# Performance work log

Measured on AMD Instinct MI355X. Metric: run time of the kernel, lower is better.

The kernel has to match this reference:

```python
import jax, jax.numpy as jnp
import numpy as np

HEADS = 16
DIM_HEAD = 64
EPS = 1e-8
MASK_VALUE = -np.finfo(np.float32).max


def rotate_half(x):
    # x: [..., rot_dim]; split into two halves (j=2 grouping) and rotate
    x1, x2 = jnp.split(x.reshape(*x.shape[:-1], 2, x.shape[-1] // 2), 2, axis=-2)
    x1 = x1.squeeze(-2)
    x2 = x2.squeeze(-2)
    return jnp.concatenate((-x2, x1), axis=-1)


def apply_rotary_pos_emb(t, freqs):
    # t: [b, h, n, d], freqs: [n, rot_dim]
    rot_dim = freqs.shape[-1]
    t_rot, t_pass = t[..., :rot_dim], t[..., rot_dim:]
    t_rot = t_rot * jnp.cos(freqs) + rotate_half(t_rot) * jnp.sin(freqs)
    return jnp.concatenate((t_rot, t_pass), axis=-1)


def setup_inputs() -> dict:
    key = jax.random.key(0)
    ks = jax.random.split(key, 6)
    b, n, dim = 2, 2048, 1024
    inner = HEADS * DIM_HEAD
    rot_dim = 32
    return {
        "x": jax.random.normal(ks[0], (b, n, dim), jnp.float32),
        "freqs": jax.random.normal(ks[1], (n, rot_dim), jnp.float32),
        "gamma": jnp.ones((dim,), jnp.float32),
        "Wq": jax.random.normal(ks[2], (dim, inner), jnp.float32) * (dim ** -0.5),
        "Wkv": jax.random.normal(ks[3], (dim, 2 * inner), jnp.float32) * (dim ** -0.5),
        "Wo": jax.random.normal(ks[4], (inner, dim), jnp.float32) * (inner ** -0.5),
        "bo": jnp.zeros((dim,), jnp.float32),
    }


def reference(x, freqs, gamma, Wq, Wkv, Wo, bo):
    b, n, dim = x.shape
    scale = DIM_HEAD ** -0.5

    # RMSNorm (norm-based formulation, matching the torch code)
    norm = jnp.linalg.norm(x, axis=-1, keepdims=True) * (dim ** -0.5)
    xn = x / jnp.maximum(norm, EPS) * gamma

    q = xn @ Wq                      # [b, n, h*d]
    kv = xn @ Wkv                    # [b, n, 2*h*d]
    k, v = jnp.split(kv, 2, axis=-1)

    def to_heads(t):
        return t.reshape(b, n, HEADS, DIM_HEAD).transpose(0, 2, 1, 3)  # [b,h,n,d]

    q, k, v = map(to_heads, (q, k, v))
    q = q * scale

    q = apply_rotary_pos_emb(q, freqs)
    k = apply_rotary_pos_emb(k, freqs)

    sim = jnp.einsum('bhid,bhjd->bhij', q, k)
    causal_mask = jnp.triu(jnp.ones((n, n), bool), k=1)
    sim = jnp.where(causal_mask, MASK_VALUE, sim)

    attn = jax.nn.softmax(sim, axis=-1)
    out = jnp.einsum('bhij,bhjd->bhid', attn, v)
    out = out.transpose(0, 2, 1, 3).reshape(b, n, HEADS * DIM_HEAD)
    return out @ Wo + bo
```

## Files before the change

### kernel.cpp

```cpp
#include <hip/hip_runtime.h>
#include <hip/hip_bf16.h>
#include <math.h>

typedef short s8 __attribute__((ext_vector_type(8)));
typedef float f4 __attribute__((ext_vector_type(4)));

#define HEADS 16
#define DHEAD 64
#define NSEQ 2048
#define BATCH 2
#define DIM 1024
#define ROT 32

static __device__ __forceinline__ unsigned short f2bf(float f) {
    union { float f; unsigned int u; } v; v.f = f;
    unsigned int u = v.u;
    unsigned int r = (u + 0x7FFFu + ((u >> 16) & 1u)) >> 16;
    return (unsigned short)r;
}

static __device__ __forceinline__ unsigned int cvt_pk_bf16(float lo, float hi) {
    unsigned int r;
    asm volatile("v_cvt_pk_bf16_f32 %0, %1, %2" : "=v"(r) : "v"(lo), "v"(hi));
    return r;
}

static __device__ __forceinline__ void gload_lds16(
        const unsigned short* g, unsigned short* l) {
    __builtin_amdgcn_global_load_lds(
        (const __attribute__((address_space(1))) void*)g,
        (__attribute__((address_space(3))) void*)l,
        16, 0, 0);
}

__global__ __launch_bounds__(256) void transpose_f32_bf16(
        const float* __restrict__ in, unsigned short* __restrict__ out,
        int K, int N) {
    __shared__ float tile[32][33];
    int n0 = blockIdx.x * 32, k0 = blockIdx.y * 32;
    int tx = threadIdx.x, ty = threadIdx.y;
    #pragma unroll
    for (int j = 0; j < 32; j += 8)
        tile[ty + j][tx] = in[(size_t)(k0 + ty + j) * N + n0 + tx];
    __syncthreads();
    #pragma unroll
    for (int j = 0; j < 32; j += 8)
        out[(size_t)(n0 + ty + j) * K + k0 + tx] = f2bf(tile[tx][ty + j]);
}

__global__ __launch_bounds__(256) void freqs_prep(
        const float* __restrict__ freqs, float* __restrict__ cs) {
    int i = blockIdx.x * 256 + threadIdx.x;
    int npos = i >> 6, j = i & 63;
    int q = j >> 4;
    int fi = (q >> 1) * 16 + (j & 15);
    float f = freqs[npos * ROT + fi];
    cs[i] = (q & 1) ? sinf(f) : cosf(f);
}

__global__ __launch_bounds__(256) void rmsnorm_kernel(
        const float* __restrict__ x, const float* __restrict__ gamma,
        unsigned short* __restrict__ xn) {
    int row = blockIdx.x;
    int tid = threadIdx.x;
    float4 v = ((const float4*)(x + (size_t)row * DIM))[tid];
    float ss = v.x * v.x + v.y * v.y + v.z * v.z + v.w * v.w;
    #pragma unroll
    for (int m = 1; m < 64; m <<= 1) ss += __shfl_xor(ss, m, 64);
    __shared__ float wsum[4];
    int wave = tid >> 6;
    if ((tid & 63) == 0) wsum[wave] = ss;
    __syncthreads();
    float total = wsum[0] + wsum[1] + wsum[2] + wsum[3];
    float norm = sqrtf(total * (1.0f / DIM));
    float inv = 1.0f / fmaxf(norm, 1e-8f);
    float4 g = ((const float4*)gamma)[tid];
    ushort4 o;
    o.x = f2bf(v.x * inv * g.x);
    o.y = f2bf(v.y * inv * g.y);
    o.z = f2bf(v.z * inv * g.z);
    o.w = f2bf(v.w * inv * g.w);
    ((ushort4*)(xn + (size_t)row * DIM))[tid] = o;
}

static __device__ __forceinline__ void gemm_core64(
        const unsigned short* __restrict__ A, const unsigned short* __restrict__ BT,
        int bm0, int bn0, unsigned short* As, unsigned short* Bs, f4 acc[2][4]) {
    const int Kd = DIM;
    int tid = threadIdx.x, lane = tid & 63, w = tid >> 6;
    int wr = w >> 1, wc = w & 1;
    int r16 = lane & 15, g8 = 8 * (lane >> 4);
    int srow = lane >> 2, scol = (lane & 3) * 8;
    const unsigned short* Ag0 = A  + (size_t)(bm0 + w * 16 + srow) * Kd + scol;
    const unsigned short* Bg0 = BT + (size_t)(bn0 + (w * 2 + 0) * 16 + srow) * Kd + scol;
    const unsigned short* Bg1 = BT + (size_t)(bn0 + (w * 2 + 1) * 16 + srow) * Kd + scol;
    unsigned short* Al  = As + w * 512;
    unsigned short* Bl0 = Bs + (w * 2 + 0) * 512;
    unsigned short* Bl1 = Bs + (w * 2 + 1) * 512;
    const unsigned short* ar = As + (wr * 32 + r16) * 32 + g8;
    const unsigned short* br = Bs + (wc * 64 + r16) * 32 + g8;
    for (int k0 = 0; k0 < Kd; k0 += 32) {
        gload_lds16(Ag0 + k0, Al);
        gload_lds16(Bg0 + k0, Bl0);
        gload_lds16(Bg1 + k0, Bl1);
        __syncthreads();
        s8 a0 = *(const s8*)(ar);
        s8 a1 = *(const s8*)(ar + 512);
        s8 b0 = *(const s8*)(br);
        s8 b1 = *(const s8*)(br + 512);
        s8 b2 = *(const s8*)(br + 1024);
        s8 b3 = *(const s8*)(br + 1536);
        acc[0][0] = __builtin_amdgcn_mfma_f32_16x16x32_bf16(a0, b0, acc[0][0], 0, 0, 0);
        acc[0][1] = __builtin_amdgcn_mfma_f32_16x16x32_bf16(a0, b1, acc[0][1], 0, 0, 0);
        acc[0][2] = __builtin_amdgcn_mfma_f32_16x16x32_bf16(a0, b2, acc[0][2], 0, 0, 0);
        acc[0][3] = __builtin_amdgcn_mfma_f32_16x16x32_bf16(a0, b3, acc[0][3], 0, 0, 0);
        acc[1][0] = __builtin_amdgcn_mfma_f32_16x16x32_bf16(a1, b0, acc[1][0], 0, 0, 0);
        acc[1][1] = __builtin_amdgcn_mfma_f32_16x16x32_bf16(a1, b1, acc[1][1], 0, 0, 0);
        acc[1][2] = __builtin_amdgcn_mfma_f32_16x16x32_bf16(a1, b2, acc[1][2], 0, 0, 0);
        acc[1][3] = __builtin_amdgcn_mfma_f32_16x16x32_bf16(a1, b3, acc[1][3], 0, 0, 0);
        __syncthreads();
    }
}

__global__ __launch_bounds__(256) void gemm_q(
        const unsigned short* __restrict__ xn, const unsigned short* __restrict__ WqT,
        const float* __restrict__ cs, unsigned short* __restrict__ q_h) {
    __shared__ unsigned short As[64 * 32];
    __shared__ unsigned short Bs[128 * 32];
    f4 acc[2][4];
    #pragma unroll
    for (int m = 0; m < 2; ++m)
        #pragma unroll
        for (int n = 0; n < 4; ++n) acc[m][n] = 0.f;
    int bm0 = blockIdx.y * 64, bn0 = blockIdx.x * 128;
    gemm_core64(xn, WqT, bm0, bn0, As, Bs, acc);
    int lane = threadIdx.x & 63, w = threadIdx.x >> 6;
    int wr = w >> 1, wc = w & 1, g = lane >> 4, c0 = lane & 15;
    int h = 2 * blockIdx.x + wc;
    #pragma unroll
    for (int m = 0; m < 2; ++m)
        #pragma unroll
        for (int r = 0; r < 4; ++r) {
            int row = bm0 + wr * 32 + m * 16 + 4 * g + r;
            int b = row >> 11, npos = row & 2047;
            const float* csr = cs + npos * 64;
            float a0 = acc[m][0][r] * 0.125f;
            float a1 = acc[m][1][r] * 0.125f;
            float q0 = a0 * csr[c0] - a1 * csr[16 + c0];
            float q1 = a1 * csr[32 + c0] + a0 * csr[48 + c0];
            unsigned short* dst = q_h + ((size_t)(b * HEADS + h) * NSEQ + npos) * DHEAD;
            dst[c0]      = f2bf(q0);
            dst[16 + c0] = f2bf(q1);
            dst[32 + c0] = f2bf(acc[m][2][r] * 0.125f);
            dst[48 + c0] = f2bf(acc[m][3][r] * 0.125f);
        }
}

__global__ __launch_bounds__(256) void gemm_kv(
        const unsigned short* __restrict__ xn, const unsigned short* __restrict__ WkvT,
        const float* __restrict__ cs, unsigned short* __restrict__ k_h,
        unsigned short* __restrict__ v_t) {
    __shared__ unsigned short As[64 * 32];
    __shared__ unsigned short Bs[128 * 32];
    f4 acc[2][4];
    #pragma unroll
    for (int m = 0; m < 2; ++m)
        #pragma unroll
        for (int n = 0; n < 4; ++n) acc[m][n] = 0.f;
    int bm0 = blockIdx.y * 64, bn0 = blockIdx.x * 128;
    gemm_core64(xn, WkvT, bm0, bn0, As, Bs, acc);
    int lane = threadIdx.x & 63, w = threadIdx.x >> 6;
    int wr = w >> 1, wc = w & 1, g = lane >> 4, c0 = lane & 15;
    bool is_k = (blockIdx.x < 8);
    int h = 2 * (blockIdx.x & 7) + wc;
    if (is_k) {
        #pragma unroll
        for (int m = 0; m < 2; ++m)
            #pragma unroll
            for (int r = 0; r < 4; ++r) {
                int row = bm0 + wr * 32 + m * 16 + 4 * g + r;
                int b = row >> 11, npos = row & 2047;
                const float* csr = cs + npos * 64;
                float a0 = acc[m][0][r], a1 = acc[m][1][r];
                float k0v = a0 * csr[c0] - a1 * csr[16 + c0];
                float k1v = a1 * csr[32 + c0] + a0 * csr[48 + c0];
                unsigned short* dst = k_h + ((size_t)(b * HEADS + h) * NSEQ + npos) * DHEAD;
                dst[c0]      = f2bf(k0v);
                dst[16 + c0] = f2bf(k1v);
                dst[32 + c0] = f2bf(acc[m][2][r]);
                dst[48 + c0] = f2bf(acc[m][3][r]);
            }
    } else {
        #pragma unroll
        for (int m = 0; m < 2; ++m) {
            int row0 = bm0 + wr * 32 + m * 16 + 4 * g;
            int b = row0 >> 11, npos0 = row0 & 2047;
            unsigned short* vb = v_t + (size_t)(b * HEADS + h) * DHEAD * NSEQ;
            #pragma unroll
            for (int n = 0; n < 4; ++n) {
                uint2 pk;
                pk.x = cvt_pk_bf16(acc[m][n][0], acc[m][n][1]);
                pk.y = cvt_pk_bf16(acc[m][n][2], acc[m][n][3]);
                *(uint2*)(vb + (size_t)(n * 16 + c0) * NSEQ + npos0) = pk;
            }
        }
    }
}

#define PSTRIDE 72

static __device__ __forceinline__ void stage_kv64(
        const unsigned short* __restrict__ kb, const unsigned short* __restrict__ vb,
        int j0, unsigned short* Kd, unsigned short* Vd, int w, int lane) {
    int r8 = lane >> 3, c = lane & 7;
    int sc = c ^ r8;
    #pragma unroll
    for (int i = 0; i < 2; ++i) {
        int rb = (w * 2 + i) * 8;
        int r = rb + r8;
        gload_lds16(kb + (size_t)(j0 + r) * DHEAD + sc * 8, Kd + rb * DHEAD);
        gload_lds16(vb + (size_t)r * NSEQ + j0 + sc * 8,    Vd + rb * DHEAD);
    }
}

template<bool MASKT>
static __device__ __forceinline__ void attn_tile_lds(
        int j0, int q0, int g, int c0, int njt,
        const unsigned short* Kc, const unsigned short* Vc,
        s8 qf0, s8 qf1, unsigned short* plw,
        f4 o[4], float& m, float& l) {
    int sw = c0 & 7;
    int off0 = ((g ^ sw) << 3);
    int off1 = (((g + 4) ^ sw) << 3);
    f4 s[4];
    #pragma unroll
    for (int jt = 0; jt < 4; ++jt) {
        f4 acc; acc = 0.f;
        if (!MASKT || jt < njt) {
            const unsigned short* kp = Kc + (jt * 16 + c0) * DHEAD;
            s8 kf0 = *(const s8*)(kp + off0);
            s8 kf1 = *(const s8*)(kp + off1);
            acc = __builtin_amdgcn_mfma_f32_16x16x32_bf16(kf0, qf0, acc, 0, 0, 0);
            acc = __builtin_amdgcn_mfma_f32_16x16x32_bf16(kf1, qf1, acc, 0, 0, 0);
        }
        s[jt] = acc;
    }
    if (MASKT) {
        #pragma unroll
        for (int jt = 0; jt < 4; ++jt)
            #pragma unroll
            for (int r = 0; r < 4; ++r) {
                int j = j0 + jt * 16 + 4 * g + r;
                if (j > q0 + c0) s[jt][r] = -1e30f;
            }
    }
    f4 mv = s[0];
    #pragma unroll
    for (int jt = 1; jt < 4; ++jt)
        #pragma unroll
        for (int r = 0; r < 4; ++r) mv[r] = fmaxf(mv[r], s[jt][r]);
    float mx = fmaxf(fmaxf(mv[0], mv[1]), fmaxf(mv[2], mv[3]));
    mx = fmaxf(mx, __shfl_xor(mx, 16));
    mx = fmaxf(mx, __shfl_xor(mx, 32));
    if (__any(mx > m + 8.f)) {
        float mnew = fmaxf(m, mx);
        float alpha = __expf(m - mnew);
        l *= alpha;
        #pragma unroll
        for (int dc = 0; dc < 4; ++dc)
            #pragma unroll
            for (int r = 0; r < 4; ++r) o[dc][r] *= alpha;
        m = mnew;
    }
    float rs = 0.f;
    unsigned int* prow = (unsigned int*)(plw + c0 * PSTRIDE);
    #pragma unroll
    for (int jt = 0; jt < 4; ++jt) {
        f4 p;
        #pragma unroll
        for (int r = 0; r < 4; ++r) { p[r] = __expf(s[jt][r] - m); rs += p[r]; }
        uint2 pk;
        pk.x = cvt_pk_bf16(p[0], p[1]);
        pk.y = cvt_pk_bf16(p[2], p[3]);
        ((uint2*)prow)[jt * 4 + g] = pk;
    }
    rs += __shfl_xor(rs, 16);
    rs += __shfl_xor(rs, 32);
    l += rs;
    __builtin_amdgcn_sched_barrier(0);
    asm volatile("s_waitcnt lgkmcnt(0)" ::: "memory");
    __builtin_amdgcn_sched_barrier(0);
    const unsigned short* prd = plw + c0 * PSTRIDE + 8 * g;
    s8 pf0 = *(const s8*)(prd);
    s8 pf1 = *(const s8*)(prd + 32);
    bool hi_half = (!MASKT) || (njt > 2);
    #pragma unroll
    for (int dc = 0; dc < 4; ++dc) {
        const unsigned short* vp = Vc + (dc * 16 + c0) * DHEAD;
        s8 vf0 = *(const s8*)(vp + off0);
        o[dc] = __builtin_amdgcn_mfma_f32_16x16x32_bf16(vf0, pf0, o[dc], 0, 0, 0);
        if (hi_half) {
            s8 vf1 = *(const s8*)(vp + off1);
            o[dc] = __builtin_amdgcn_mfma_f32_16x16x32_bf16(vf1, pf1, o[dc], 0, 0, 0);
        }
    }
}

__global__ __launch_bounds__(256) void attn_kernel(
        const unsigned short* __restrict__ q_h, const unsigned short* __restrict__ k_h,
        const unsigned short* __restrict__ v_t, unsigned short* __restrict__ attn_out) {
    __shared__ unsigned short Ks[2][64 * DHEAD];
    __shared__ unsigned short Vs[2][64 * DHEAD];
    __shared__ unsigned short p_lds[4][16][PSTRIDE];
    int tid = threadIdx.x, lane = tid & 63, w = tid >> 6;
    int g = lane >> 4, c0 = lane & 15;
    int bid = blockIdx.x;
    int x = (bid >> 3) & 15;
    int bh = (bid & 7) + ((bid >> 7) << 3);
    const unsigned short* qb = q_h + (size_t)bh * NSEQ * DHEAD;
    const unsigned short* kb = k_h + (size_t)bh * NSEQ * DHEAD;
    const unsigned short* vb = v_t + (size_t)bh * DHEAD * NSEQ;
    unsigned short* plw = &p_lds[w][0][0];
    int b = bh >> 4, h = bh & 15;
    for (int pass = 0; pass < 2; ++pass) {
        int qt = pass ? (31 - x) : x;
        int q0 = qt * 64 + w * 16;
        s8 qf0 = *(const s8*)(qb + (size_t)(q0 + c0) * DHEAD + 8 * g);
        s8 qf1 = *(const s8*)(qb + (size_t)(q0 + c0) * DHEAD + 32 + 8 * g);
        f4 o[4]; o[0] = 0.f; o[1] = 0.f; o[2] = 0.f; o[3] = 0.f;
        float m = -1e30f, l = 0.f;
        int nt = qt + 1;
        stage_kv64(kb, vb, 0, Ks[0], Vs[0], w, lane);
        __syncthreads();
        for (int t = 0; t < nt; ++t) {
            const unsigned short* Kc = Ks[t & 1];
            const unsigned short* Vc = Vs[t & 1];
            if (t + 1 < nt)
                stage_kv64(kb, vb, (t + 1) * 64, Ks[(t + 1) & 1], Vs[(t + 1) & 1], w, lane);
            if (t == nt - 1)
                attn_tile_lds<true>(t * 64, q0, g, c0, w + 1, Kc, Vc, qf0, qf1, plw, o, m, l);
            else
                attn_tile_lds<false>(t * 64, q0, g, c0, 4, Kc, Vc, qf0, qf1, plw, o, m, l);
            __syncthreads();
        }
        float invl = 1.0f / l;
        unsigned short* dst = attn_out + ((size_t)(b * NSEQ) + q0 + c0) * (HEADS * DHEAD) + h * DHEAD;
        #pragma unroll
        for (int dc = 0; dc < 4; ++dc) {
            uint2 pk;
            pk.x = cvt_pk_bf16(o[dc][0] * invl, o[dc][1] * invl);
            pk.y = cvt_pk_bf16(o[dc][2] * invl, o[dc][3] * invl);
            *(uint2*)(dst + dc * 16 + 4 * g) = pk;
        }
    }
}

__global__ __launch_bounds__(256) void gemm_o(
        const unsigned short* __restrict__ attn, const unsigned short* __restrict__ WoT,
        const float* __restrict__ bo, float* __restrict__ out) {
    __shared__ unsigned short As[64 * 32];
    __shared__ unsigned short Bs[128 * 32];
    f4 acc[2][4];
    #pragma unroll
    for (int m = 0; m < 2; ++m)
        #pragma unroll
        for (int n = 0; n < 4; ++n) acc[m][n] = 0.f;
    int bm0 = blockIdx.y * 64, bn0 = blockIdx.x * 128;
    gemm_core64(attn, WoT, bm0, bn0, As, Bs, acc);
    int lane = threadIdx.x & 63, w = threadIdx.x >> 6;
    int wr = w >> 1, wc = w & 1, g = lane >> 4, c0 = lane & 15;
    #pragma unroll
    for (int m = 0; m < 2; ++m)
        #pragma unroll
        for (int r = 0; r < 4; ++r) {
            int row = bm0 + wr * 32 + m * 16 + 4 * g + r;
            #pragma unroll
            for (int n = 0; n < 4; ++n) {
                int col = bn0 + wc * 64 + n * 16 + c0;
                out[(size_t)row * DIM + col] = acc[m][n][r] + bo[col];
            }
        }
}

extern "C" void kernel_launch(void* const* d_in, const int* in_sizes, int n_in,
                              void* d_out, int out_size, void* d_ws, size_t ws_size,
                              hipStream_t stream) {
    const float* x     = (const float*)d_in[0];
    const float* freqs = (const float*)d_in[1];
    const float* gamma = (const float*)d_in[2];
    const float* Wq    = (const float*)d_in[3];
    const float* Wkv   = (const float*)d_in[4];
    const float* Wo    = (const float*)d_in[5];
    const float* bo    = (const float*)d_in[6];
    float* out = (float*)d_out;

    char* ws = (char*)d_ws;
    unsigned short* xn   = (unsigned short*)(ws + 0);
    unsigned short* WqT  = (unsigned short*)(ws + 8388608);
    unsigned short* WkvT = (unsigned short*)(ws + 10485760);
    unsigned short* WoT  = (unsigned short*)(ws + 14680064);
    unsigned short* q_h  = (unsigned short*)(ws + 16777216);
    unsigned short* k_h  = (unsigned short*)(ws + 25165824);
    unsigned short* v_t  = (unsigned short*)(ws + 33554432);
    float*          cs   = (float*)(ws + 41943040);
    unsigned short* attn = xn;

    dim3 tb(32, 8);
    transpose_f32_bf16<<<dim3(32, 32), tb, 0, stream>>>(Wq,  WqT,  1024, 1024);
    transpose_f32_bf16<<<dim3(64, 32), tb, 0, stream>>>(Wkv, WkvT, 1024, 2048);
    transpose_f32_bf16<<<dim3(32, 32), tb, 0, stream>>>(Wo,  WoT,  1024, 1024);
    freqs_prep<<<512, 256, 0, stream>>>(freqs, cs);
    rmsnorm_kernel<<<4096, 256, 0, stream>>>(x, gamma, xn);
    gemm_q <<<dim3(8, 64),  256, 0, stream>>>(xn, WqT, cs, q_h);
    gemm_kv<<<dim3(16, 64), 256, 0, stream>>>(xn, WkvT, cs, k_h, v_t);
    attn_kernel<<<512, 256, 0, stream>>>(q_h, k_h, v_t, attn);
    gemm_o <<<dim3(8, 64),  256, 0, stream>>>(attn, WoT, bo, out);
}
```

Measured before the change: 139.0 us.

## Use 128x128 GEMM tiles, exp2 softmax with folded log2e, one q-tile per attention block

```diff
diff --git a/kernel.cpp b/kernel.cpp
--- a/kernel.cpp
+++ b/kernel.cpp
@@ -11,6 +11,7 @@
 #define BATCH 2
 #define DIM 1024
 #define ROT 32
+#define QSCALE 0.18033688011112042f
 
 static __device__ __forceinline__ unsigned short f2bf(float f) {
     union { float f; unsigned int u; } v; v.f = f;
@@ -83,41 +84,40 @@
     ((ushort4*)(xn + (size_t)row * DIM))[tid] = o;
 }
 
-static __device__ __forceinline__ void gemm_core64(
+static __device__ __forceinline__ void gemm_core128(
         const unsigned short* __restrict__ A, const unsigned short* __restrict__ BT,
-        int bm0, int bn0, unsigned short* As, unsigned short* Bs, f4 acc[2][4]) {
+        int bm0, int bn0, unsigned short* As, unsigned short* Bs, f4 acc[4][4]) {
     const int Kd = DIM;
     int tid = threadIdx.x, lane = tid & 63, w = tid >> 6;
     int wr = w >> 1, wc = w & 1;
     int r16 = lane & 15, g8 = 8 * (lane >> 4);
-    int srow = lane >> 2, scol = (lane & 3) * 8;
-    const unsigned short* Ag0 = A  + (size_t)(bm0 + w * 16 + srow) * Kd + scol;
-    const unsigned short* Bg0 = BT + (size_t)(bn0 + (w * 2 + 0) * 16 + srow) * Kd + scol;
-    const unsigned short* Bg1 = BT + (size_t)(bn0 + (w * 2 + 1) * 16 + srow) * Kd + scol;
-    unsigned short* Al  = As + w * 512;
-    unsigned short* Bl0 = Bs + (w * 2 + 0) * 512;
-    unsigned short* Bl1 = Bs + (w * 2 + 1) * 512;
-    const unsigned short* ar = As + (wr * 32 + r16) * 32 + g8;
+    int sr = lane >> 2, sc = (lane & 3) * 8;
+    const unsigned short* Ag0 = A  + (size_t)(bm0 +      w * 16 + sr) * Kd + sc;
+    const unsigned short* Ag1 = A  + (size_t)(bm0 + 64 + w * 16 + sr) * Kd + sc;
+    const unsigned short* Bg0 = BT + (size_t)(bn0 +      w * 16 + sr) * Kd + sc;
+    const unsigned short* Bg1 = BT + (size_t)(bn0 + 64 + w * 16 + sr) * Kd + sc;
+    unsigned short* Al0 = As + (w * 16) * 32;
+    unsigned short* Al1 = As + (64 + w * 16) * 32;
+    unsigned short* Bl0 = Bs + (w * 16) * 32;
+    unsigned short* Bl1 = Bs + (64 + w * 16) * 32;
+    const unsigned short* ar = As + (wr * 64 + r16) * 32 + g8;
     const unsigned short* br = Bs + (wc * 64 + r16) * 32 + g8;
     for (int k0 = 0; k0 < Kd; k0 += 32) {
-        gload_lds16(Ag0 + k0, Al);
+        gload_lds16(Ag0 + k0, Al0);
+        gload_lds16(Ag1 + k0, Al1);
         gload_lds16(Bg0 + k0, Bl0);
         gload_lds16(Bg1 + k0, Bl1);
         __syncthreads();
-        s8 a0 = *(const s8*)(ar);
-        s8 a1 = *(const s8*)(ar + 512);
-        s8 b0 = *(const s8*)(br);
-        s8 b1 = *(const s8*)(br + 512);
-        s8 b2 = *(const s8*)(br + 1024);
-        s8 b3 = *(const s8*)(br + 1536);
-        acc[0][0] = __builtin_amdgcn_mfma_f32_16x16x32_bf16(a0, b0, acc[0][0], 0, 0, 0);
-        acc[0][1] = __builtin_amdgcn_mfma_f32_16x16x32_bf16(a0, b1, acc[0][1], 0, 0, 0);
-        acc[0][2] = __builtin_amdgcn_mfma_f32_16x16x32_bf16(a0, b2, acc[0][2], 0, 0, 0);
-        acc[0][3] = __builtin_amdgcn_mfma_f32_16x16x32_bf16(a0, b3, acc[0][3], 0, 0, 0);
-        acc[1][0] = __builtin_amdgcn_mfma_f32_16x16x32_bf16(a1, b0, acc[1][0], 0, 0, 0);
-        acc[1][1] = __builtin_amdgcn_mfma_f32_16x16x32_bf16(a1, b1, acc[1][1], 0, 0, 0);
-        acc[1][2] = __builtin_amdgcn_mfma_f32_16x16x32_bf16(a1, b2, acc[1][2], 0, 0, 0);
-        acc[1][3] = __builtin_amdgcn_mfma_f32_16x16x32_bf16(a1, b3, acc[1][3], 0, 0, 0);
+        s8 a[4], b[4];
+        #pragma unroll
+        for (int m = 0; m < 4; ++m) a[m] = *(const s8*)(ar + m * 512);
+        #pragma unroll
+        for (int n = 0; n < 4; ++n) b[n] = *(const s8*)(br + n * 512);
+        #pragma unroll
+        for (int m = 0; m < 4; ++m)
+            #pragma unroll
+            for (int n = 0; n < 4; ++n)
+                acc[m][n] = __builtin_amdgcn_mfma_f32_16x16x32_bf16(a[m], b[n], acc[m][n], 0, 0, 0);
         __syncthreads();
     }
 }
@@ -125,34 +125,34 @@
 __global__ __launch_bounds__(256) void gemm_q(
         const unsigned short* __restrict__ xn, const unsigned short* __restrict__ WqT,
         const float* __restrict__ cs, unsigned short* __restrict__ q_h) {
-    __shared__ unsigned short As[64 * 32];
+    __shared__ unsigned short As[128 * 32];
     __shared__ unsigned short Bs[128 * 32];
-    f4 acc[2][4];
-    #pragma unroll
-    for (int m = 0; m < 2; ++m)
+    f4 acc[4][4];
+    #pragma unroll
+    for (int m = 0; m < 4; ++m)
         #pragma unroll
         for (int n = 0; n < 4; ++n) acc[m][n] = 0.f;
-    int bm0 = blockIdx.y * 64, bn0 = blockIdx.x * 128;
-    gemm_core64(xn, WqT, bm0, bn0, As, Bs, acc);
+    int bm0 = blockIdx.y * 128, bn0 = blockIdx.x * 128;
+    gemm_core128(xn, WqT, bm0, bn0, As, Bs, acc);
     int lane = threadIdx.x & 63, w = threadIdx.x >> 6;
     int wr = w >> 1, wc = w & 1, g = lane >> 4, c0 = lane & 15;
     int h = 2 * blockIdx.x + wc;
     #pragma unroll
-    for (int m = 0; m < 2; ++m)
+    for (int m = 0; m < 4; ++m)
         #pragma unroll
         for (int r = 0; r < 4; ++r) {
-            int row = bm0 + wr * 32 + m * 16 + 4 * g + r;
+            int row = bm0 + wr * 64 + m * 16 + 4 * g + r;
             int b = row >> 11, npos = row & 2047;
             const float* csr = cs + npos * 64;
-            float a0 = acc[m][0][r] * 0.125f;
-            float a1 = acc[m][1][r] * 0.125f;
+            float a0 = acc[m][0][r] * QSCALE;
+            float a1 = acc[m][1][r] * QSCALE;
             float q0 = a0 * csr[c0] - a1 * csr[16 + c0];
             float q1 = a1 * csr[32 + c0] + a0 * csr[48 + c0];
             unsigned short* dst = q_h + ((size_t)(b * HEADS + h) * NSEQ + npos) * DHEAD;
             dst[c0]      = f2bf(q0);
             dst[16 + c0] = f2bf(q1);
-            dst[32 + c0] = f2bf(acc[m][2][r] * 0.125f);
-            dst[48 + c0] = f2bf(acc[m][3][r] * 0.125f);
+            dst[32 + c0] = f2bf(acc[m][2][r] * QSCALE);
+            dst[48 + c0] = f2bf(acc[m][3][r] * QSCALE);
         }
 }
 
@@ -160,25 +160,25 @@
         const unsigned short* __restrict__ xn, const unsigned short* __restrict__ WkvT,
         const float* __restrict__ cs, unsigned short* __restrict__ k_h,
         unsigned short* __restrict__ v_t) {
-    __shared__ unsigned short As[64 * 32];
+    __shared__ unsigned short As[128 * 32];
     __shared__ unsigned short Bs[128 * 32];
-    f4 acc[2][4];
-    #pragma unroll
-    for (int m = 0; m < 2; ++m)
+    f4 acc[4][4];
+    #pragma unroll
+    for (int m = 0; m < 4; ++m)
         #pragma unroll
         for (int n = 0; n < 4; ++n) acc[m][n] = 0.f;
-    int bm0 = blockIdx.y * 64, bn0 = blockIdx.x * 128;
-    gemm_core64(xn, WkvT, bm0, bn0, As, Bs, acc);
+    int bm0 = blockIdx.y * 128, bn0 = blockIdx.x * 128;
+    gemm_core128(xn, WkvT, bm0, bn0, As, Bs, acc);
     int lane = threadIdx.x & 63, w = threadIdx.x >> 6;
     int wr = w >> 1, wc = w & 1, g = lane >> 4, c0 = lane & 15;
     bool is_k = (blockIdx.x < 8);
     int h = 2 * (blockIdx.x & 7) + wc;
     if (is_k) {
         #pragma unroll
-        for (int m = 0; m < 2; ++m)
+        for (int m = 0; m < 4; ++m)
             #pragma unroll
             for (int r = 0; r < 4; ++r) {
-                int row = bm0 + wr * 32 + m * 16 + 4 * g + r;
+                int row = bm0 + wr * 64 + m * 16 + 4 * g + r;
                 int b = row >> 11, npos = row & 2047;
                 const float* csr = cs + npos * 64;
                 float a0 = acc[m][0][r], a1 = acc[m][1][r];
@@ -192,8 +192,8 @@
             }
     } else {
         #pragma unroll
-        for (int m = 0; m < 2; ++m) {
-            int row0 = bm0 + wr * 32 + m * 16 + 4 * g;
+        for (int m = 0; m < 4; ++m) {
+            int row0 = bm0 + wr * 64 + m * 16 + 4 * g;
             int b = row0 >> 11, npos0 = row0 & 2047;
             unsigned short* vb = v_t + (size_t)(b * HEADS + h) * DHEAD * NSEQ;
             #pragma unroll
@@ -262,9 +262,9 @@
     float mx = fmaxf(fmaxf(mv[0], mv[1]), fmaxf(mv[2], mv[3]));
     mx = fmaxf(mx, __shfl_xor(mx, 16));
     mx = fmaxf(mx, __shfl_xor(mx, 32));
-    if (__any(mx > m + 8.f)) {
+    if (__any(mx > m + 11.5f)) {
         float mnew = fmaxf(m, mx);
-        float alpha = __expf(m - mnew);
+        float alpha = exp2f(m - mnew);
         l *= alpha;
         #pragma unroll
         for (int dc = 0; dc < 4; ++dc)
@@ -278,7 +278,7 @@
     for (int jt = 0; jt < 4; ++jt) {
         f4 p;
         #pragma unroll
-        for (int r = 0; r < 4; ++r) { p[r] = __expf(s[jt][r] - m); rs += p[r]; }
+        for (int r = 0; r < 4; ++r) { p[r] = exp2f(s[jt][r] - m); rs += p[r]; }
         uint2 pk;
         pk.x = cvt_pk_bf16(p[0], p[1]);
         pk.y = cvt_pk_bf16(p[2], p[3]);
@@ -315,65 +315,63 @@
     int tid = threadIdx.x, lane = tid & 63, w = tid >> 6;
     int g = lane >> 4, c0 = lane & 15;
     int bid = blockIdx.x;
-    int x = (bid >> 3) & 15;
-    int bh = (bid & 7) + ((bid >> 7) << 3);
+    int k = bid >> 3;
+    int qt = 31 - (k & 31);
+    int bh = (bid & 7) + ((k >> 5) << 3);
     const unsigned short* qb = q_h + (size_t)bh * NSEQ * DHEAD;
     const unsigned short* kb = k_h + (size_t)bh * NSEQ * DHEAD;
     const unsigned short* vb = v_t + (size_t)bh * DHEAD * NSEQ;
     unsigned short* plw = &p_lds[w][0][0];
     int b = bh >> 4, h = bh & 15;
-    for (int pass = 0; pass < 2; ++pass) {
-        int qt = pass ? (31 - x) : x;
-        int q0 = qt * 64 + w * 16;
-        s8 qf0 = *(const s8*)(qb + (size_t)(q0 + c0) * DHEAD + 8 * g);
-        s8 qf1 = *(const s8*)(qb + (size_t)(q0 + c0) * DHEAD + 32 + 8 * g);
-        f4 o[4]; o[0] = 0.f; o[1] = 0.f; o[2] = 0.f; o[3] = 0.f;
-        float m = -1e30f, l = 0.f;
-        int nt = qt + 1;
-        stage_kv64(kb, vb, 0, Ks[0], Vs[0], w, lane);
+    int q0 = qt * 64 + w * 16;
+    s8 qf0 = *(const s8*)(qb + (size_t)(q0 + c0) * DHEAD + 8 * g);
+    s8 qf1 = *(const s8*)(qb + (size_t)(q0 + c0) * DHEAD + 32 + 8 * g);
+    f4 o[4]; o[0] = 0.f; o[1] = 0.f; o[2] = 0.f; o[3] = 0.f;
+    float m = -1e30f, l = 0.f;
+    int nt = qt + 1;
+    stage_kv64(kb, vb, 0, Ks[0], Vs[0], w, lane);
+    __syncthreads();
+    for (int t = 0; t < nt; ++t) {
+        const unsigned short* Kc = Ks[t & 1];
+        const unsigned short* Vc = Vs[t & 1];
+        if (t + 1 < nt)
+            stage_kv64(kb, vb, (t + 1) * 64, Ks[(t + 1) & 1], Vs[(t + 1) & 1], w, lane);
+        if (t == nt - 1)
+            attn_tile_lds<true>(t * 64, q0, g, c0, w + 1, Kc, Vc, qf0, qf1, plw, o, m, l);
+        else
+            attn_tile_lds<false>(t * 64, q0, g, c0, 4, Kc, Vc, qf0, qf1, plw, o, m, l);
         __syncthreads();
-        for (int t = 0; t < nt; ++t) {
-            const unsigned short* Kc = Ks[t & 1];
-            const unsigned short* Vc = Vs[t & 1];
-            if (t + 1 < nt)
-                stage_kv64(kb, vb, (t + 1) * 64, Ks[(t + 1) & 1], Vs[(t + 1) & 1], w, lane);
-            if (t == nt - 1)
-                attn_tile_lds<true>(t * 64, q0, g, c0, w + 1, Kc, Vc, qf0, qf1, plw, o, m, l);
-            else
-                attn_tile_lds<false>(t * 64, q0, g, c0, 4, Kc, Vc, qf0, qf1, plw, o, m, l);
-            __syncthreads();
-        }
-        float invl = 1.0f / l;
-        unsigned short* dst = attn_out + ((size_t)(b * NSEQ) + q0 + c0) * (HEADS * DHEAD) + h * DHEAD;
-        #pragma unroll
-        for (int dc = 0; dc < 4; ++dc) {
-            uint2 pk;
-            pk.x = cvt_pk_bf16(o[dc][0] * invl, o[dc][1] * invl);
-            pk.y = cvt_pk_bf16(o[dc][2] * invl, o[dc][3] * invl);
-            *(uint2*)(dst + dc * 16 + 4 * g) = pk;
-        }
+    }
+    float invl = 1.0f / l;
+    unsigned short* dst = attn_out + ((size_t)(b * NSEQ) + q0 + c0) * (HEADS * DHEAD) + h * DHEAD;
+    #pragma unroll
+    for (int dc = 0; dc < 4; ++dc) {
+        uint2 pk;
+        pk.x = cvt_pk_bf16(o[dc][0] * invl, o[dc][1] * invl);
+        pk.y = cvt_pk_bf16(o[dc][2] * invl, o[dc][3] * invl);
+        *(uint2*)(dst + dc * 16 + 4 * g) = pk;
     }
 }
 
 __global__ __launch_bounds__(256) void gemm_o(
         const unsigned short* __restrict__ attn, const unsigned short* __restrict__ WoT,
         const float* __restrict__ bo, float* __restrict__ out) {
-    __shared__ unsigned short As[64 * 32];
+    __shared__ unsigned short As[128 * 32];
     __shared__ unsigned short Bs[128 * 32];
-    f4 acc[2][4];
-    #pragma unroll
-    for (int m = 0; m < 2; ++m)
+    f4 acc[4][4];
+    #pragma unroll
+    for (int m = 0; m < 4; ++m)
         #pragma unroll
         for (int n = 0; n < 4; ++n) acc[m][n] = 0.f;
-    int bm0 = blockIdx.y * 64, bn0 = blockIdx.x * 128;
-    gemm_core64(attn, WoT, bm0, bn0, As, Bs, acc);
+    int bm0 = blockIdx.y * 128, bn0 = blockIdx.x * 128;
+    gemm_core128(attn, WoT, bm0, bn0, As, Bs, acc);
     int lane = threadIdx.x & 63, w = threadIdx.x >> 6;
     int wr = w >> 1, wc = w & 1, g = lane >> 4, c0 = lane & 15;
     #pragma unroll
-    for (int m = 0; m < 2; ++m)
+    for (int m = 0; m < 4; ++m)
         #pragma unroll
         for (int r = 0; r < 4; ++r) {
-            int row = bm0 + wr * 32 + m * 16 + 4 * g + r;
+            int row = bm0 + wr * 64 + m * 16 + 4 * g + r;
             #pragma unroll
             for (int n = 0; n < 4; ++n) {
                 int col = bn0 + wc * 64 + n * 16 + c0;
@@ -411,8 +409,8 @@
     transpose_f32_bf16<<<dim3(32, 32), tb, 0, stream>>>(Wo,  WoT,  1024, 1024);
     freqs_prep<<<512, 256, 0, stream>>>(freqs, cs);
     rmsnorm_kernel<<<4096, 256, 0, stream>>>(x, gamma, xn);
-    gemm_q <<<dim3(8, 64),  256, 0, stream>>>(xn, WqT, cs, q_h);
-    gemm_kv<<<dim3(16, 64), 256, 0, stream>>>(xn, WkvT, cs, k_h, v_t);
-    attn_kernel<<<512, 256, 0, stream>>>(q_h, k_h, v_t, attn);
-    gemm_o <<<dim3(8, 64),  256, 0, stream>>>(attn, WoT, bo, out);
-}
+    gemm_q <<<dim3(8, 32),  256, 0, stream>>>(xn, WqT, cs, q_h);
+    gemm_kv<<<dim3(16, 32), 256, 0, stream>>>(xn, WkvT, cs, k_h, v_t);
+    attn_kernel<<<1024, 256, 0, stream>>>(q_h, k_h, v_t, attn);
+    gemm_o <<<dim3(8, 32),  256, 0, stream>>>(attn, WoT, bo, out);
+}
```

Result: slower. 167.1 us (+20.2%).

## Fuse prep kernels and QKV GEMMs, use exp2 softmax, split attention blocks

Applied to the files above, without the earlier changes.

```diff
diff --git a/kernel.cpp b/kernel.cpp
--- a/kernel.cpp
+++ b/kernel.cpp
@@ -11,6 +11,7 @@
 #define BATCH 2
 #define DIM 1024
 #define ROT 32
+#define QSCALE 0.18033688011112042f
 
 static __device__ __forceinline__ unsigned short f2bf(float f) {
     union { float f; unsigned int u; } v; v.f = f;
@@ -33,29 +34,42 @@
         16, 0, 0);
 }
 
-__global__ __launch_bounds__(256) void transpose_f32_bf16(
+static __device__ __forceinline__ void tr_tile(
         const float* __restrict__ in, unsigned short* __restrict__ out,
-        int K, int N) {
-    __shared__ float tile[32][33];
-    int n0 = blockIdx.x * 32, k0 = blockIdx.y * 32;
-    int tx = threadIdx.x, ty = threadIdx.y;
+        int K, int N, int n0, int k0, int tid, float* tile ) {
+    int tx = tid & 31, ty = tid >> 5;
     #pragma unroll
     for (int j = 0; j < 32; j += 8)
-        tile[ty + j][tx] = in[(size_t)(k0 + ty + j) * N + n0 + tx];
+        tile[(ty + j) * 33 + tx] = in[(size_t)(k0 + ty + j) * N + n0 + tx];
     __syncthreads();
     #pragma unroll
     for (int j = 0; j < 32; j += 8)
-        out[(size_t)(n0 + ty + j) * K + k0 + tx] = f2bf(tile[tx][ty + j]);
-}
-
-__global__ __launch_bounds__(256) void freqs_prep(
-        const float* __restrict__ freqs, float* __restrict__ cs) {
-    int i = blockIdx.x * 256 + threadIdx.x;
-    int npos = i >> 6, j = i & 63;
-    int q = j >> 4;
-    int fi = (q >> 1) * 16 + (j & 15);
-    float f = freqs[npos * ROT + fi];
-    cs[i] = (q & 1) ? sinf(f) : cosf(f);
+        out[(size_t)(n0 + ty + j) * K + k0 + tx] = f2bf(tile[tx * 33 + ty + j]);
+}
+
+__global__ __launch_bounds__(256) void prep_kernel(
+        const float* __restrict__ Wq, const float* __restrict__ Wkv,
+        const float* __restrict__ Wo, const float* __restrict__ freqs,
+        unsigned short* __restrict__ WqT, unsigned short* __restrict__ WkvT,
+        unsigned short* __restrict__ WoT, float* __restrict__ cs) {
+    __shared__ float tile[32 * 33];
+    int bid = blockIdx.x, tid = threadIdx.x;
+    if (bid < 1024) {
+        tr_tile(Wq, WqT, 1024, 1024, (bid & 31) * 32, (bid >> 5) * 32, tid, tile);
+    } else if (bid < 3072) {
+        int idx = bid - 1024;
+        tr_tile(Wkv, WkvT, 1024, 2048, (idx & 63) * 32, (idx >> 6) * 32, tid, tile);
+    } else if (bid < 4096) {
+        int idx = bid - 3072;
+        tr_tile(Wo, WoT, 1024, 1024, (idx & 31) * 32, (idx >> 5) * 32, tid, tile);
+    } else {
+        int i = (bid - 4096) * 256 + tid;
+        int npos = i >> 6, j = i & 63;
+        int q = j >> 4;
+        int fi = (q >> 1) * 16 + (j & 15);
+        float f = freqs[npos * ROT + fi];
+        cs[i] = (q & 1) ? sinf(f) : cosf(f);
+    }
 }
 
 __global__ __launch_bounds__(256) void rmsnorm_kernel(
@@ -122,43 +136,10 @@
     }
 }
 
-__global__ __launch_bounds__(256) void gemm_q(
+__global__ __launch_bounds__(256) void gemm_qkv(
         const unsigned short* __restrict__ xn, const unsigned short* __restrict__ WqT,
-        const float* __restrict__ cs, unsigned short* __restrict__ q_h) {
-    __shared__ unsigned short As[64 * 32];
-    __shared__ unsigned short Bs[128 * 32];
-    f4 acc[2][4];
-    #pragma unroll
-    for (int m = 0; m < 2; ++m)
-        #pragma unroll
-        for (int n = 0; n < 4; ++n) acc[m][n] = 0.f;
-    int bm0 = blockIdx.y * 64, bn0 = blockIdx.x * 128;
-    gemm_core64(xn, WqT, bm0, bn0, As, Bs, acc);
-    int lane = threadIdx.x & 63, w = threadIdx.x >> 6;
-    int wr = w >> 1, wc = w & 1, g = lane >> 4, c0 = lane & 15;
-    int h = 2 * blockIdx.x + wc;
-    #pragma unroll
-    for (int m = 0; m < 2; ++m)
-        #pragma unroll
-        for (int r = 0; r < 4; ++r) {
-            int row = bm0 + wr * 32 + m * 16 + 4 * g + r;
-            int b = row >> 11, npos = row & 2047;
-            const float* csr = cs + npos * 64;
-            float a0 = acc[m][0][r] * 0.125f;
-            float a1 = acc[m][1][r] * 0.125f;
-            float q0 = a0 * csr[c0] - a1 * csr[16 + c0];
-            float q1 = a1 * csr[32 + c0] + a0 * csr[48 + c0];
-            unsigned short* dst = q_h + ((size_t)(b * HEADS + h) * NSEQ + npos) * DHEAD;
-            dst[c0]      = f2bf(q0);
-            dst[16 + c0] = f2bf(q1);
-            dst[32 + c0] = f2bf(acc[m][2][r] * 0.125f);
-            dst[48 + c0] = f2bf(acc[m][3][r] * 0.125f);
-        }
-}
-
-__global__ __launch_bounds__(256) void gemm_kv(
-        const unsigned short* __restrict__ xn, const unsigned short* __restrict__ WkvT,
-        const float* __restrict__ cs, unsigned short* __restrict__ k_h,
+        const unsigned short* __restrict__ WkvT, const float* __restrict__ cs,
+        unsigned short* __restrict__ q_h, unsigned short* __restrict__ k_h,
         unsigned short* __restrict__ v_t) {
     __shared__ unsigned short As[64 * 32];
     __shared__ unsigned short Bs[128 * 32];
@@ -167,13 +148,34 @@
     for (int m = 0; m < 2; ++m)
         #pragma unroll
         for (int n = 0; n < 4; ++n) acc[m][n] = 0.f;
-    int bm0 = blockIdx.y * 64, bn0 = blockIdx.x * 128;
-    gemm_core64(xn, WkvT, bm0, bn0, As, Bs, acc);
+    int bx = blockIdx.x;
+    bool isq = (bx < 8);
+    int bm0 = blockIdx.y * 64;
+    int bn0 = (isq ? bx : (bx - 8)) * 128;
+    gemm_core64(xn, isq ? WqT : WkvT, bm0, bn0, As, Bs, acc);
     int lane = threadIdx.x & 63, w = threadIdx.x >> 6;
     int wr = w >> 1, wc = w & 1, g = lane >> 4, c0 = lane & 15;
-    bool is_k = (blockIdx.x < 8);
-    int h = 2 * (blockIdx.x & 7) + wc;
-    if (is_k) {
+    if (isq) {
+        int h = 2 * bx + wc;
+        #pragma unroll
+        for (int m = 0; m < 2; ++m)
+            #pragma unroll
+            for (int r = 0; r < 4; ++r) {
+                int row = bm0 + wr * 32 + m * 16 + 4 * g + r;
+                int b = row >> 11, npos = row & 2047;
+                const float* csr = cs + npos * 64;
+                float a0 = acc[m][0][r] * QSCALE;
+                float a1 = acc[m][1][r] * QSCALE;
+                float q0 = a0 * csr[c0] - a1 * csr[16 + c0];
+                float q1 = a1 * csr[32 + c0] + a0 * csr[48 + c0];
+                unsigned short* dst = q_h + ((size_t)(b * HEADS + h) * NSEQ + npos) * DHEAD;
+                dst[c0]      = f2bf(q0);
+                dst[16 + c0] = f2bf(q1);
+                dst[32 + c0] = f2bf(acc[m][2][r] * QSCALE);
+                dst[48 + c0] = f2bf(acc[m][3][r] * QSCALE);
+            }
+    } else if (bx < 16) {
+        int h = 2 * (bx - 8) + wc;
         #pragma unroll
         for (int m = 0; m < 2; ++m)
             #pragma unroll
@@ -191,6 +193,7 @@
                 dst[48 + c0] = f2bf(acc[m][3][r]);
             }
     } else {
+        int h = 2 * (bx - 16) + wc;
         #pragma unroll
         for (int m = 0; m < 2; ++m) {
             int row0 = bm0 + wr * 32 + m * 16 + 4 * g;
@@ -262,9 +265,9 @@
     float mx = fmaxf(fmaxf(mv[0], mv[1]), fmaxf(mv[2], mv[3]));
     mx = fmaxf(mx, __shfl_xor(mx, 16));
     mx = fmaxf(mx, __shfl_xor(mx, 32));
-    if (__any(mx > m + 8.f)) {
+    if (__any(mx > m + 11.5f)) {
         float mnew = fmaxf(m, mx);
-        float alpha = __expf(m - mnew);
+        float alpha = exp2f(m - mnew);
         l *= alpha;
         #pragma unroll
         for (int dc = 0; dc < 4; ++dc)
@@ -278,7 +281,7 @@
     for (int jt = 0; jt < 4; ++jt) {
         f4 p;
         #pragma unroll
-        for (int r = 0; r < 4; ++r) { p[r] = __expf(s[jt][r] - m); rs += p[r]; }
+        for (int r = 0; r < 4; ++r) { p[r] = exp2f(s[jt][r] - m); rs += p[r]; }
         uint2 pk;
         pk.x = cvt_pk_bf16(p[0], p[1]);
         pk.y = cvt_pk_bf16(p[2], p[3]);
@@ -315,43 +318,41 @@
     int tid = threadIdx.x, lane = tid & 63, w = tid >> 6;
     int g = lane >> 4, c0 = lane & 15;
     int bid = blockIdx.x;
-    int x = (bid >> 3) & 15;
-    int bh = (bid & 7) + ((bid >> 7) << 3);
+    int k = bid >> 3;
+    int qt = 31 - (k >> 2);
+    int bh = (bid & 7) + ((k & 3) << 3);
     const unsigned short* qb = q_h + (size_t)bh * NSEQ * DHEAD;
     const unsigned short* kb = k_h + (size_t)bh * NSEQ * DHEAD;
     const unsigned short* vb = v_t + (size_t)bh * DHEAD * NSEQ;
     unsigned short* plw = &p_lds[w][0][0];
     int b = bh >> 4, h = bh & 15;
-    for (int pass = 0; pass < 2; ++pass) {
-        int qt = pass ? (31 - x) : x;
-        int q0 = qt * 64 + w * 16;
-        s8 qf0 = *(const s8*)(qb + (size_t)(q0 + c0) * DHEAD + 8 * g);
-        s8 qf1 = *(const s8*)(qb + (size_t)(q0 + c0) * DHEAD + 32 + 8 * g);
-        f4 o[4]; o[0] = 0.f; o[1] = 0.f; o[2] = 0.f; o[3] = 0.f;
-        float m = -1e30f, l = 0.f;
-        int nt = qt + 1;
-        stage_kv64(kb, vb, 0, Ks[0], Vs[0], w, lane);
+    int q0 = qt * 64 + w * 16;
+    s8 qf0 = *(const s8*)(qb + (size_t)(q0 + c0) * DHEAD + 8 * g);
+    s8 qf1 = *(const s8*)(qb + (size_t)(q0 + c0) * DHEAD + 32 + 8 * g);
+    f4 o[4]; o[0] = 0.f; o[1] = 0.f; o[2] = 0.f; o[3] = 0.f;
+    float m = -1e30f, l = 0.f;
+    int nt = qt + 1;
+    stage_kv64(kb, vb, 0, Ks[0], Vs[0], w, lane);
+    __syncthreads();
+    for (int t = 0; t < nt; ++t) {
+        const unsigned short* Kc = Ks[t & 1];
+        const unsigned short* Vc = Vs[t & 1];
+        if (t + 1 < nt)
+            stage_kv64(kb, vb, (t + 1) * 64, Ks[(t + 1) & 1], Vs[(t + 1) & 1], w, lane);
+        if (t == nt - 1)
+            attn_tile_lds<true>(t * 64, q0, g, c0, w + 1, Kc, Vc, qf0, qf1, plw, o, m, l);
+        else
+            attn_tile_lds<false>(t * 64, q0, g, c0, 4, Kc, Vc, qf0, qf1, plw, o, m, l);
         __syncthreads();
-        for (int t = 0; t < nt; ++t) {
-            const unsigned short* Kc = Ks[t & 1];
-            const unsigned short* Vc = Vs[t & 1];
-            if (t + 1 < nt)
-                stage_kv64(kb, vb, (t + 1) * 64, Ks[(t + 1) & 1], Vs[(t + 1) & 1], w, lane);
-            if (t == nt - 1)
-                attn_tile_lds<true>(t * 64, q0, g, c0, w + 1, Kc, Vc, qf0, qf1, plw, o, m, l);
-            else
-                attn_tile_lds<false>(t * 64, q0, g, c0, 4, Kc, Vc, qf0, qf1, plw, o, m, l);
-            __syncthreads();
-        }
-        float invl = 1.0f / l;
-        unsigned short* dst = attn_out + ((size_t)(b * NSEQ) + q0 + c0) * (HEADS * DHEAD) + h * DHEAD;
-        #pragma unroll
-        for (int dc = 0; dc < 4; ++dc) {
-            uint2 pk;
-            pk.x = cvt_pk_bf16(o[dc][0] * invl, o[dc][1] * invl);
-            pk.y = cvt_pk_bf16(o[dc][2] * invl, o[dc][3] * invl);
-            *(uint2*)(dst + dc * 16 + 4 * g) = pk;
-        }
+    }
+    float invl = 1.0f / l;
+    unsigned short* dst = attn_out + ((size_t)(b * NSEQ) + q0 + c0) * (HEADS * DHEAD) + h * DHEAD;
+    #pragma unroll
+    for (int dc = 0; dc < 4; ++dc) {
+        uint2 pk;
+        pk.x = cvt_pk_bf16(o[dc][0] * invl, o[dc][1] * invl);
+        pk.y = cvt_pk_bf16(o[dc][2] * invl, o[dc][3] * invl);
+        *(uint2*)(dst + dc * 16 + 4 * g) = pk;
     }
 }
 
@@ -405,14 +406,9 @@
     float*          cs   = (float*)(ws + 41943040);
     unsigned short* attn = xn;
 
-    dim3 tb(32, 8);
-    transpose_f32_bf16<<<dim3(32, 32), tb, 0, stream>>>(Wq,  WqT,  1024, 1024);
-    transpose_f32_bf16<<<dim3(64, 32), tb, 0, stream>>>(Wkv, WkvT, 1024, 2048);
-    transpose_f32_bf16<<<dim3(32, 32), tb, 0, stream>>>(Wo,  WoT,  1024, 1024);
-    freqs_prep<<<512, 256, 0, stream>>>(freqs, cs);
+    prep_kernel<<<4608, 256, 0, stream>>>(Wq, Wkv, Wo, freqs, WqT, WkvT, WoT, cs);
     rmsnorm_kernel<<<4096, 256, 0, stream>>>(x, gamma, xn);
-    gemm_q <<<dim3(8, 64),  256, 0, stream>>>(xn, WqT, cs, q_h);
-    gemm_kv<<<dim3(16, 64), 256, 0, stream>>>(xn, WkvT, cs, k_h, v_t);
-    attn_kernel<<<512, 256, 0, stream>>>(q_h, k_h, v_t, attn);
-    gemm_o <<<dim3(8, 64),  256, 0, stream>>>(attn, WoT, bo, out);
-}
+    gemm_qkv<<<dim3(24, 64), 256, 0, stream>>>(xn, WqT, WkvT, cs, q_h, k_h, v_t);
+    attn_kernel<<<1024, 256, 0, stream>>>(q_h, k_h, v_t, attn);
+    gemm_o  <<<dim3(8, 64), 256, 0, stream>>>(attn, WoT, bo, out);
+}
```

Result: faster. 128.9 us (-7.2%).
